# Optimization experiments

Hardware: AMD Instinct MI355X
Metric: run time of the kernel (lower is better)

## Reference

```python
import jax, jax.numpy as jnp
import numpy as np

N = 100000
E = 1600000
IN_C, HID_C, OUT_C = 128, 128, 64
EPS = 1e-5


def setup_inputs() -> dict:
    key = jax.random.key(0)
    ks = jax.random.split(key, 12)
    x = jax.random.normal(ks[0], (N, IN_C), dtype=jnp.float32)
    edge_index = jax.random.randint(ks[1], (2, E), 0, N, dtype=jnp.int64)
    def lin(k, fan_in, fan_out):
        s = 1.0 / np.sqrt(fan_in)
        return jax.random.uniform(k, (fan_in, fan_out), jnp.float32, -s, s)
    return {
        "x": x,
        "W1": lin(ks[2], IN_C, HID_C), "b1": jnp.zeros((HID_C,), jnp.float32),
        "g1": jnp.ones((HID_C,), jnp.float32), "be1": jnp.zeros((HID_C,), jnp.float32),
        "W2": lin(ks[3], HID_C, HID_C), "b2": jnp.zeros((HID_C,), jnp.float32),
        "g2": jnp.ones((HID_C,), jnp.float32), "be2": jnp.zeros((HID_C,), jnp.float32),
        "W3": lin(ks[4], HID_C, OUT_C), "b3": jnp.zeros((OUT_C,), jnp.float32),
        "edge_index": edge_index,
    }


def gcn_conv(x, W, b, src, dst, dinv):
    # x' = D^{-1/2}(A+I)D^{-1/2} (x W) + b ; src/dst already include self loops
    h = x @ W                                    # [N, C_out]
    norm = dinv[src] * dinv[dst]                 # [E+N]
    msg = h[src] * norm[:, None]                 # [E+N, C_out] (memory-bound gather)
    out = jax.ops.segment_sum(msg, dst, num_segments=N)
    return out + b


def batchnorm_relu(h, gamma, beta):
    # training-mode BatchNorm1d: batch stats over nodes, biased variance
    mean = jnp.mean(h, axis=0)
    var = jnp.mean((h - mean) ** 2, axis=0)
    y = gamma * (h - mean) * jax.lax.rsqrt(var + EPS) + beta
    return jax.nn.relu(y)


def reference(x, W1, b1, g1, be1, W2, b2, g2, be2, W3, b3, edge_index):
    loop = jnp.arange(N, dtype=edge_index.dtype)
    src = jnp.concatenate([edge_index[0], loop])
    dst = jnp.concatenate([edge_index[1], loop])
    deg = jax.ops.segment_sum(jnp.ones_like(dst, dtype=jnp.float32), dst, num_segments=N)
    dinv = jax.lax.rsqrt(jnp.maximum(deg, 1.0))

    h = gcn_conv(x, W1, b1, src, dst, dinv)
    h = batchnorm_relu(h, g1, be1)
    h = gcn_conv(h, W2, b2, src, dst, dinv)
    h = batchnorm_relu(h, g2, be2)
    out = gcn_conv(h, W3, b3, src, dst, dinv)
    return (h, out)
```

## Files before the change

kernel.cpp:

```cpp
#include <hip/hip_runtime.h>
#include <hip/hip_bf16.h>

#define NNODES 100000
#define NEDGES 1600000
#define EPSBN 1e-5f

#define BKT_SHIFT 9
#define NODES_PER_BKT 512
#define NBKT 196
#define NCHUNK 256
#define CHUNK 6250
#define SRC_MASK 0x1FFFF
#define NSLOT 64

typedef unsigned short u16;
typedef unsigned int u32;
typedef __bf16 bf16x8 __attribute__((ext_vector_type(8)));
typedef float floatx4 __attribute__((ext_vector_type(4)));

__device__ __forceinline__ u16 f2bf(float f) {
    unsigned int u = __float_as_uint(f);
    unsigned int r = (u + 0x7fffu + ((u >> 16) & 1u)) >> 16;
    return (u16)r;
}
__device__ __forceinline__ float bflo(unsigned int u) { return __uint_as_float(u << 16); }
__device__ __forceinline__ float bfhi(unsigned int u) { return __uint_as_float(u & 0xffff0000u); }


__global__ __launch_bounds__(256) void k_hist(const int* __restrict__ ei, int* __restrict__ histT) {
    __shared__ int h[NBKT];
    int tid = threadIdx.x;
    if (tid < NBKT) h[tid] = 0;
    __syncthreads();
    int base = blockIdx.x * CHUNK;
    for (int e = base + tid; e < base + CHUNK; e += 256) {
        int d = ei[NEDGES + e];
        atomicAdd(&h[d >> BKT_SHIFT], 1);
    }
    __syncthreads();
    if (tid < NBKT) histT[tid * NCHUNK + blockIdx.x] = h[tid];
}

__global__ __launch_bounds__(256) void k_bbase(const int* __restrict__ histT, int* __restrict__ bbase,
                                               int* __restrict__ rowptr) {
    __shared__ int sdata[256];
    int tid = threadIdx.x;
    int s = 0;
    if (tid < NBKT) {
        for (int g = 0; g < NCHUNK; ++g) s += histT[tid * NCHUNK + g];
    }
    int val = s;
    sdata[tid] = val;
    __syncthreads();
    for (int off = 1; off < 256; off <<= 1) {
        int add = (tid >= off) ? sdata[tid - off] : 0;
        __syncthreads();
        val += add;
        sdata[tid] = val;
        __syncthreads();
    }
    if (tid < NBKT) bbase[tid] = val - s;
    if (tid == 0) { bbase[NBKT] = NEDGES; rowptr[NNODES] = NEDGES; }
}

__global__ __launch_bounds__(256) void k_bscan(const int* __restrict__ histT, const int* __restrict__ bbase,
                                               int* __restrict__ offT) {
    __shared__ int sdata[256];
    int b = blockIdx.x;
    int g = threadIdx.x;
    int v = histT[b * NCHUNK + g];
    int val = v;
    sdata[g] = val;
    __syncthreads();
    for (int off = 1; off < 256; off <<= 1) {
        int add = (g >= off) ? sdata[g - off] : 0;
        __syncthreads();
        val += add;
        sdata[g] = val;
        __syncthreads();
    }
    offT[b * NCHUNK + g] = bbase[b] + (val - v);
}

__global__ __launch_bounds__(256) void k_scatter(const int* __restrict__ ei, const int* __restrict__ offT,
                                                 u32* __restrict__ rec) {
    __shared__ int cur[NBKT];
    int tid = threadIdx.x;
    if (tid < NBKT) cur[tid] = offT[tid * NCHUNK + blockIdx.x];
    __syncthreads();
    int base = blockIdx.x * CHUNK;
    for (int e = base + tid; e < base + CHUNK; e += 256) {
        int s = ei[e];
        int d = ei[NEDGES + e];
        int b = d >> BKT_SHIFT;
        int p = atomicAdd(&cur[b], 1);
        rec[p] = ((u32)(d & (NODES_PER_BKT - 1)) << 17) | (u32)s;
    }
}

__global__ __launch_bounds__(256) void k_bfill(const u32* __restrict__ rec, const int* __restrict__ bbase,
                                               int* __restrict__ rowptr, float* __restrict__ dinv,
                                               int* __restrict__ colsrc) {
    __shared__ int cnt[NODES_PER_BKT];
    __shared__ int sdata[256];
    int tid = threadIdx.x;
    int b = blockIdx.x;
    int n0 = b * NODES_PER_BKT;
    int r0 = bbase[b], r1 = bbase[b + 1];
    cnt[2 * tid] = 0;
    cnt[2 * tid + 1] = 0;
    __syncthreads();
    for (int r = r0 + tid; r < r1; r += 256) {
        atomicAdd(&cnt[rec[r] >> 17], 1);
    }
    __syncthreads();
    int c0 = cnt[2 * tid], c1 = cnt[2 * tid + 1];
    int ps = c0 + c1;
    int val = ps;
    sdata[tid] = val;
    __syncthreads();
    for (int off = 1; off < 256; off <<= 1) {
        int add = (tid >= off) ? sdata[tid - off] : 0;
        __syncthreads();
        val += add;
        sdata[tid] = val;
        __syncthreads();
    }
    int e0 = val - ps;
    int e1 = e0 + c0;
    int na = n0 + 2 * tid, nb2 = n0 + 2 * tid + 1;
    if (na < NNODES) {
        rowptr[na] = r0 + e0;
        dinv[na] = rsqrtf((float)(c0 + 1));
    }
    if (nb2 < NNODES) {
        rowptr[nb2] = r0 + e1;
        dinv[nb2] = rsqrtf((float)(c1 + 1));
    }
    cnt[2 * tid] = r0 + e0;
    cnt[2 * tid + 1] = r0 + e1;
    __syncthreads();
    for (int r = r0 + tid; r < r1; r += 256) {
        u32 u = rec[r];
        int p = atomicAdd(&cnt[u >> 17], 1);
        colsrc[p] = (int)(u & SRC_MASK);
    }
}


template <int COUT>
__device__ __forceinline__ void packone(const float* __restrict__ W, u16* __restrict__ Wp, int f) {
    constexpr int CT = COUT / 16;
    if (f >= 4 * CT * 64) return;
    int ks = f / (CT * 64);
    int ct = (f / 64) % CT;
    int lane = f % 64;
    int quad = lane >> 4, mm = lane & 15;
#pragma unroll
    for (int j = 0; j < 8; ++j) {
        float v = W[(size_t)(ks * 32 + quad * 8 + j) * COUT + ct * 16 + mm];
        Wp[(size_t)f * 8 + j] = f2bf(v);
    }
}

__global__ __launch_bounds__(256) void k_packW_all(const float* __restrict__ W1, const float* __restrict__ W2,
                                                   const float* __restrict__ W3, u16* __restrict__ Wp1,
                                                   u16* __restrict__ Wp2, u16* __restrict__ Wp3) {
    int b = blockIdx.x;
    if (b < 8) packone<128>(W1, Wp1, b * 256 + threadIdx.x);
    else if (b < 16) packone<128>(W2, Wp2, (b - 8) * 256 + threadIdx.x);
    else packone<64>(W3, Wp3, (b - 16) * 256 + threadIdx.x);
}


template <int COUT, bool AFFINE, bool WRITEH, bool BF16IN>
__global__ __launch_bounds__(256) void k_mfma_gemm(const void* __restrict__ Xv, const u16* __restrict__ Wp,
                                                   const float* __restrict__ dinv,
                                                   const float* __restrict__ scale, const float* __restrict__ shift,
                                                   u16* __restrict__ Bout, float* __restrict__ Hout) {
    constexpr int CT = COUT / 16;
    const int wave = threadIdx.x >> 6;
    const int lane = threadIdx.x & 63;
    const int quad = lane >> 4;
    const int m = lane & 15;
    const int rowbase = blockIdx.x * 64 + wave * 16;
    const int arow = rowbase + m;
    const bool rv = arow < NNODES;
    floatx4 acc[CT];
#pragma unroll
    for (int ct = 0; ct < CT; ++ct) acc[ct] = floatx4{0.f, 0.f, 0.f, 0.f};
#pragma unroll
    for (int ks = 0; ks < 4; ++ks) {
        const int k0 = ks * 32 + quad * 8;
        float4 xa = make_float4(0.f, 0.f, 0.f, 0.f), xb = xa;
        if (rv) {
            if (BF16IN) {
                uint4 q = *(const uint4*)((const u16*)Xv + (size_t)arow * 128 + k0);
                xa.x = bflo(q.x); xa.y = bfhi(q.x); xa.z = bflo(q.y); xa.w = bfhi(q.y);
                xb.x = bflo(q.z); xb.y = bfhi(q.z); xb.z = bflo(q.w); xb.w = bfhi(q.w);
            } else {
                xa = *(const float4*)((const float*)Xv + (size_t)arow * 128 + k0);
                xb = *(const float4*)((const float*)Xv + (size_t)arow * 128 + k0 + 4);
            }
        }
        if (AFFINE) {
            float4 sa = *(const float4*)(scale + k0), sb = *(const float4*)(scale + k0 + 4);
            float4 ha = *(const float4*)(shift + k0), hb = *(const float4*)(shift + k0 + 4);
            xa.x = fmaxf(fmaf(xa.x, sa.x, ha.x), 0.f);
            xa.y = fmaxf(fmaf(xa.y, sa.y, ha.y), 0.f);
            xa.z = fmaxf(fmaf(xa.z, sa.z, ha.z), 0.f);
            xa.w = fmaxf(fmaf(xa.w, sa.w, ha.w), 0.f);
            xb.x = fmaxf(fmaf(xb.x, sb.x, hb.x), 0.f);
            xb.y = fmaxf(fmaf(xb.y, sb.y, hb.y), 0.f);
            xb.z = fmaxf(fmaf(xb.z, sb.z, hb.z), 0.f);
            xb.w = fmaxf(fmaf(xb.w, sb.w, hb.w), 0.f);
        }
        if (WRITEH && rv) {
            *(float4*)(Hout + (size_t)arow * 128 + k0) = xa;
            *(float4*)(Hout + (size_t)arow * 128 + k0 + 4) = xb;
        }
        union { u16 h[8]; bf16x8 v; } ua;
        ua.h[0] = f2bf(xa.x); ua.h[1] = f2bf(xa.y); ua.h[2] = f2bf(xa.z); ua.h[3] = f2bf(xa.w);
        ua.h[4] = f2bf(xb.x); ua.h[5] = f2bf(xb.y); ua.h[6] = f2bf(xb.z); ua.h[7] = f2bf(xb.w);
#pragma unroll
        for (int ct = 0; ct < CT; ++ct) {
            uint4 bv = *(const uint4*)(Wp + ((size_t)(ks * CT + ct) * 64 + lane) * 8);
            bf16x8 b = *(const bf16x8*)&bv;
            acc[ct] = __builtin_amdgcn_mfma_f32_16x16x32_bf16(ua.v, b, acc[ct], 0, 0, 0);
        }
    }
    float dv[4];
#pragma unroll
    for (int reg = 0; reg < 4; ++reg) {
        int r = rowbase + quad * 4 + reg;
        dv[reg] = (r < NNODES) ? dinv[r] : 0.f;
    }
#pragma unroll
    for (int ct = 0; ct < CT; ++ct) {
#pragma unroll
        for (int reg = 0; reg < 4; ++reg) {
            int r = rowbase + quad * 4 + reg;
            if (r < NNODES) Bout[(size_t)r * COUT + ct * 16 + m] = f2bf(dv[reg] * acc[ct][reg]);
        }
    }
}


template <bool STATS, bool OUTB>
__global__ __launch_bounds__(256) void k_agg128v(const u16* __restrict__ Bm, const float* __restrict__ dinv,
                                                 const int* __restrict__ rowptr, const int* __restrict__ colsrc,
                                                 const float* __restrict__ bias, void* __restrict__ Outv,
                                                 float* __restrict__ slots) {
    __shared__ float sO[4][128];
    const int wave = threadIdx.x >> 6;
    const int node = blockIdx.x * 4 + wave;
    const int lane = threadIdx.x & 63;
    const int g = lane >> 4;
    const int c16 = lane & 15;
    const uint4* Bq = (const uint4*)Bm;
    float a0[8], a1[8];
#pragma unroll
    for (int j = 0; j < 8; ++j) { a0[j] = 0.f; a1[j] = 0.f; }
    const int beg = rowptr[node];
    const int L = rowptr[node + 1] - beg + 1;
    for (int it = 0; it < L; it += 8) {
        int i0 = it + g, i1 = it + 4 + g;
        float w0 = (i0 < L) ? 1.f : 0.f;
        float w1 = (i1 < L) ? 1.f : 0.f;
        i0 = min(i0, L - 1);
        i1 = min(i1, L - 1);
        int s0 = colsrc[beg + max(i0, 1) - 1];
        int s1 = colsrc[beg + max(i1, 1) - 1];
        if (i0 == 0) s0 = node;
        uint4 q0 = Bq[(size_t)s0 * 16 + c16];
        uint4 q1 = Bq[(size_t)s1 * 16 + c16];
        a0[0] += w0 * bflo(q0.x); a0[1] += w0 * bfhi(q0.x);
        a0[2] += w0 * bflo(q0.y); a0[3] += w0 * bfhi(q0.y);
        a0[4] += w0 * bflo(q0.z); a0[5] += w0 * bfhi(q0.z);
        a0[6] += w0 * bflo(q0.w); a0[7] += w0 * bfhi(q0.w);
        a1[0] += w1 * bflo(q1.x); a1[1] += w1 * bfhi(q1.x);
        a1[2] += w1 * bflo(q1.y); a1[3] += w1 * bfhi(q1.y);
        a1[4] += w1 * bflo(q1.z); a1[5] += w1 * bfhi(q1.z);
        a1[6] += w1 * bflo(q1.w); a1[7] += w1 * bfhi(q1.w);
    }
    const float dv = dinv[node];
    float o[8];
#pragma unroll
    for (int j = 0; j < 8; ++j) {
        float s = a0[j] + a1[j];
        s += __shfl_xor(s, 16);
        s += __shfl_xor(s, 32);
        o[j] = dv * s + bias[c16 * 8 + j];
    }
    if (g == 0) {
        if (OUTB) {
            u16* OutB = (u16*)Outv;
            union { u32 w[4]; uint4 q; } p;
            p.w[0] = (u32)f2bf(o[0]) | ((u32)f2bf(o[1]) << 16);
            p.w[1] = (u32)f2bf(o[2]) | ((u32)f2bf(o[3]) << 16);
            p.w[2] = (u32)f2bf(o[4]) | ((u32)f2bf(o[5]) << 16);
            p.w[3] = (u32)f2bf(o[6]) | ((u32)f2bf(o[7]) << 16);
            *(uint4*)(OutB + (size_t)node * 128 + c16 * 8) = p.q;
        } else {
            float* Out = (float*)Outv;
            *(float4*)(Out + (size_t)node * 128 + c16 * 8) = make_float4(o[0], o[1], o[2], o[3]);
            *(float4*)(Out + (size_t)node * 128 + c16 * 8 + 4) = make_float4(o[4], o[5], o[6], o[7]);
        }
        if (STATS) {
#pragma unroll
            for (int j = 0; j < 8; ++j) sO[wave][c16 * 8 + j] = o[j];
        }
    }
    if (STATS) {
        __syncthreads();
        if (threadIdx.x < 128) {
            float s = 0.f, q = 0.f;
#pragma unroll
            for (int wv = 0; wv < 4; ++wv) {
                float v = sO[wv][threadIdx.x];
                s += v;
                q += v * v;
            }
            float* slot = slots + (size_t)(blockIdx.x & (NSLOT - 1)) * 256;
            atomicAdd(&slot[threadIdx.x], s);
            atomicAdd(&slot[128 + threadIdx.x], q);
        }
    }
}

__global__ __launch_bounds__(256) void k_agg64v(const u16* __restrict__ Bm, const float* __restrict__ dinv,
                                                const int* __restrict__ rowptr, const int* __restrict__ colsrc,
                                                const float* __restrict__ bias, float* __restrict__ Out) {
    const int node = blockIdx.x * 4 + (threadIdx.x >> 6);
    const int lane = threadIdx.x & 63;
    const int g = lane >> 3;
    const int c8 = lane & 7;
    const uint4* Bq = (const uint4*)Bm;
    float a0[8], a1[8];
#pragma unroll
    for (int j = 0; j < 8; ++j) { a0[j] = 0.f; a1[j] = 0.f; }
    const int beg = rowptr[node];
    const int L = rowptr[node + 1] - beg + 1;
    for (int it = 0; it < L; it += 16) {
        int i0 = it + g, i1 = it + 8 + g;
        float w0 = (i0 < L) ? 1.f : 0.f;
        float w1 = (i1 < L) ? 1.f : 0.f;
        i0 = min(i0, L - 1);
        i1 = min(i1, L - 1);
        int s0 = colsrc[beg + max(i0, 1) - 1];
        int s1 = colsrc[beg + max(i1, 1) - 1];
        if (i0 == 0) s0 = node;
        uint4 q0 = Bq[(size_t)s0 * 8 + c8];
        uint4 q1 = Bq[(size_t)s1 * 8 + c8];
        a0[0] += w0 * bflo(q0.x); a0[1] += w0 * bfhi(q0.x);
        a0[2] += w0 * bflo(q0.y); a0[3] += w0 * bfhi(q0.y);
        a0[4] += w0 * bflo(q0.z); a0[5] += w0 * bfhi(q0.z);
        a0[6] += w0 * bflo(q0.w); a0[7] += w0 * bfhi(q0.w);
        a1[0] += w1 * bflo(q1.x); a1[1] += w1 * bfhi(q1.x);
        a1[2] += w1 * bflo(q1.y); a1[3] += w1 * bfhi(q1.y);
        a1[4] += w1 * bflo(q1.z); a1[5] += w1 * bfhi(q1.z);
        a1[6] += w1 * bflo(q1.w); a1[7] += w1 * bfhi(q1.w);
    }
    const float dv = dinv[node];
    float o[8];
#pragma unroll
    for (int j = 0; j < 8; ++j) {
        float s = a0[j] + a1[j];
        s += __shfl_xor(s, 8);
        s += __shfl_xor(s, 16);
        s += __shfl_xor(s, 32);
        o[j] = dv * s + bias[c8 * 8 + j];
    }
    if (g == 0) {
        float4 v0 = make_float4(o[0], o[1], o[2], o[3]);
        float4 v1 = make_float4(o[4], o[5], o[6], o[7]);
        *(float4*)(Out + (size_t)node * 64 + c8 * 8) = v0;
        *(float4*)(Out + (size_t)node * 64 + c8 * 8 + 4) = v1;
    }
}


__global__ void k_bn_final(const float* __restrict__ slots, const float* __restrict__ g,
                           const float* __restrict__ be, float* __restrict__ scale, float* __restrict__ shift) {
    int c = threadIdx.x;
    float s = 0.f, q = 0.f;
    for (int k = 0; k < NSLOT; ++k) {
        s += slots[(size_t)k * 256 + c];
        q += slots[(size_t)k * 256 + 128 + c];
    }
    float mean = s * (1.0f / NNODES);
    float var = q * (1.0f / NNODES) - mean * mean;
    float istd = rsqrtf(var + EPSBN);
    float sc = g[c] * istd;
    scale[c] = sc;
    shift[c] = be[c] - sc * mean;
}


extern "C" void kernel_launch(void* const* d_in, const int* in_sizes, int n_in,
                              void* d_out, int out_size, void* d_ws, size_t ws_size,
                              hipStream_t stream) {
    const float* x   = (const float*)d_in[0];
    const float* W1  = (const float*)d_in[1];
    const float* b1  = (const float*)d_in[2];
    const float* g1  = (const float*)d_in[3];
    const float* be1 = (const float*)d_in[4];
    const float* W2  = (const float*)d_in[5];
    const float* b2  = (const float*)d_in[6];
    const float* g2  = (const float*)d_in[7];
    const float* be2 = (const float*)d_in[8];
    const float* W3  = (const float*)d_in[9];
    const float* b3  = (const float*)d_in[10];
    const int* ei    = (const int*)d_in[11];

    float* out_h = (float*)d_out;
    float* out_o = (float*)d_out + (size_t)NNODES * 128;

    char* w = (char*)d_ws;
    u16* A16 = (u16*)w;        w += (size_t)NNODES * 128 * 2;
    u16* Bm = (u16*)w;         w += (size_t)NNODES * 128 * 2;
    float* dinv = (float*)w;   w += (size_t)NNODES * 4;
    int* rowptr = (int*)w;     w += (size_t)(NNODES + 32) * 4;
    int* colsrc = (int*)w;     w += (size_t)(NEDGES + 8) * 4;
    int* bbase = (int*)w;      w += (NBKT + 4) * 4;
    float* slots1 = (float*)w; w += (size_t)NSLOT * 256 * 4;
    float* slots2 = (float*)w; w += (size_t)NSLOT * 256 * 4;
    float* scale = (float*)w;  w += 128 * 4;
    float* shift = (float*)w;  w += 128 * 4;
    u16* Wp1 = (u16*)w;        w += 128 * 128 * 2;
    u16* Wp2 = (u16*)w;        w += 128 * 128 * 2;
    u16* Wp3 = (u16*)w;        w += 128 * 64 * 2;

    u32* rec  = (u32*)A16;
    int* histT = (int*)Bm;
    int* offT  = (int*)Bm + NBKT * NCHUNK;

    hipMemsetAsync(slots1, 0, (size_t)2 * NSLOT * 256 * 4, stream);

    k_packW_all<<<20, 256, 0, stream>>>(W1, W2, W3, Wp1, Wp2, Wp3);

    k_hist<<<NCHUNK, 256, 0, stream>>>(ei, histT);
    k_bbase<<<1, 256, 0, stream>>>(histT, bbase, rowptr);
    k_bscan<<<NBKT, 256, 0, stream>>>(histT, bbase, offT);
    k_scatter<<<NCHUNK, 256, 0, stream>>>(ei, offT, rec);
    k_bfill<<<NBKT, 256, 0, stream>>>(rec, bbase, rowptr, dinv, colsrc);

    const int GB = (NNODES + 63) / 64;
    const int AB = NNODES / 4;

    k_mfma_gemm<128, false, false, false><<<GB, 256, 0, stream>>>(x, Wp1, dinv, nullptr, nullptr, Bm, nullptr);
    k_agg128v<true, true><<<AB, 256, 0, stream>>>(Bm, dinv, rowptr, colsrc, b1, A16, slots1);
    k_bn_final<<<1, 128, 0, stream>>>(slots1, g1, be1, scale, shift);

    k_mfma_gemm<128, true, false, true><<<GB, 256, 0, stream>>>(A16, Wp2, dinv, scale, shift, Bm, nullptr);
    k_agg128v<true, true><<<AB, 256, 0, stream>>>(Bm, dinv, rowptr, colsrc, b2, A16, slots2);
    k_bn_final<<<1, 128, 0, stream>>>(slots2, g2, be2, scale, shift);

    k_mfma_gemm<64, true, true, true><<<GB, 256, 0, stream>>>(A16, Wp3, dinv, scale, shift, Bm, out_h);
    k_agg64v<<<AB, 256, 0, stream>>>(Bm, dinv, rowptr, colsrc, b3, out_o);
}
```

Baseline: 452.6 us.

## Pre-sort edges by source bucket before destination bucketing for gather locality

Adds a first counting-sort pass that buckets edges by source node into an intermediate (src,dst) pair array, then runs the existing destination bucketing over that array. Because the destination scatter is stable per chunk, each node's CSR neighbor list ends up roughly ordered by source, which should make the feature-row gathers in the aggregation kernels more cache-local. It costs four extra kernel launches and an extra pass of edge reads and writes over an 8-byte-per-edge staging buffer.

```diff
diff --git a/kernel.cpp b/kernel.cpp
--- a/kernel.cpp
+++ b/kernel.cpp
@@ -27,14 +27,65 @@
 __device__ __forceinline__ float bfhi(unsigned int u) { return __uint_as_float(u & 0xffff0000u); }
 
 
-__global__ __launch_bounds__(256) void k_hist(const int* __restrict__ ei, int* __restrict__ histT) {
+__global__ __launch_bounds__(256) void k_histS(const int* __restrict__ ei, int* __restrict__ histS) {
     __shared__ int h[NBKT];
     int tid = threadIdx.x;
     if (tid < NBKT) h[tid] = 0;
     __syncthreads();
     int base = blockIdx.x * CHUNK;
     for (int e = base + tid; e < base + CHUNK; e += 256) {
+        int s = ei[e];
+        atomicAdd(&h[s >> BKT_SHIFT], 1);
+    }
+    __syncthreads();
+    if (tid < NBKT) histS[tid * NCHUNK + blockIdx.x] = h[tid];
+}
+
+__global__ __launch_bounds__(256) void k_bbaseS(const int* __restrict__ histS, int* __restrict__ bbaseS) {
+    __shared__ int sdata[256];
+    int tid = threadIdx.x;
+    int s = 0;
+    if (tid < NBKT) {
+        for (int g = 0; g < NCHUNK; ++g) s += histS[tid * NCHUNK + g];
+    }
+    int val = s;
+    sdata[tid] = val;
+    __syncthreads();
+    for (int off = 1; off < 256; off <<= 1) {
+        int add = (tid >= off) ? sdata[tid - off] : 0;
+        __syncthreads();
+        val += add;
+        sdata[tid] = val;
+        __syncthreads();
+    }
+    if (tid < NBKT) bbaseS[tid] = val - s;
+}
+
+__global__ __launch_bounds__(256) void k_scatterS(const int* __restrict__ ei, const int* __restrict__ offS,
+                                                  uint2* __restrict__ est) {
+    __shared__ int cur[NBKT];
+    int tid = threadIdx.x;
+    if (tid < NBKT) cur[tid] = offS[tid * NCHUNK + blockIdx.x];
+    __syncthreads();
+    int base = blockIdx.x * CHUNK;
+    for (int e = base + tid; e < base + CHUNK; e += 256) {
+        int s = ei[e];
         int d = ei[NEDGES + e];
+        int b = s >> BKT_SHIFT;
+        int p = atomicAdd(&cur[b], 1);
+        est[p] = make_uint2((u32)s, (u32)d);
+    }
+}
+
+
+__global__ __launch_bounds__(256) void k_hist(const uint2* __restrict__ est, int* __restrict__ histT) {
+    __shared__ int h[NBKT];
+    int tid = threadIdx.x;
+    if (tid < NBKT) h[tid] = 0;
+    __syncthreads();
+    int base = blockIdx.x * CHUNK;
+    for (int e = base + tid; e < base + CHUNK; e += 256) {
+        int d = (int)est[e].y;
         atomicAdd(&h[d >> BKT_SHIFT], 1);
     }
     __syncthreads();
@@ -82,7 +133,7 @@
     offT[b * NCHUNK + g] = bbase[b] + (val - v);
 }
 
-__global__ __launch_bounds__(256) void k_scatter(const int* __restrict__ ei, const int* __restrict__ offT,
+__global__ __launch_bounds__(256) void k_scatter(const uint2* __restrict__ est, const int* __restrict__ offT,
                                                  u32* __restrict__ rec) {
     __shared__ int cur[NBKT];
     int tid = threadIdx.x;
@@ -90,8 +141,9 @@
     __syncthreads();
     int base = blockIdx.x * CHUNK;
     for (int e = base + tid; e < base + CHUNK; e += 256) {
-        int s = ei[e];
-        int d = ei[NEDGES + e];
+        uint2 p2 = est[e];
+        int s = (int)p2.x;
+        int d = (int)p2.y;
         int b = d >> BKT_SHIFT;
         int p = atomicAdd(&cur[b], 1);
         rec[p] = ((u32)(d & (NODES_PER_BKT - 1)) << 17) | (u32)s;
@@ -423,6 +475,7 @@
     int* rowptr = (int*)w;     w += (size_t)(NNODES + 32) * 4;
     int* colsrc = (int*)w;     w += (size_t)(NEDGES + 8) * 4;
     int* bbase = (int*)w;      w += (NBKT + 4) * 4;
+    int* bbaseS = (int*)w;     w += (NBKT + 4) * 4;
     float* slots1 = (float*)w; w += (size_t)NSLOT * 256 * 4;
     float* slots2 = (float*)w; w += (size_t)NSLOT * 256 * 4;
     float* scale = (float*)w;  w += 128 * 4;
@@ -432,17 +485,25 @@
     u16* Wp3 = (u16*)w;        w += 128 * 64 * 2;
 
     u32* rec  = (u32*)A16;
+    uint2* est = (uint2*)((char*)A16 + (size_t)NEDGES * 4);
     int* histT = (int*)Bm;
-    int* offT  = (int*)Bm + NBKT * NCHUNK;
+    int* offT  = histT + NBKT * NCHUNK;
+    int* histS = offT + NBKT * NCHUNK;
+    int* offS  = histS + NBKT * NCHUNK;
 
     hipMemsetAsync(slots1, 0, (size_t)2 * NSLOT * 256 * 4, stream);
 
     k_packW_all<<<20, 256, 0, stream>>>(W1, W2, W3, Wp1, Wp2, Wp3);
 
-    k_hist<<<NCHUNK, 256, 0, stream>>>(ei, histT);
+    k_histS<<<NCHUNK, 256, 0, stream>>>(ei, histS);
+    k_bbaseS<<<1, 256, 0, stream>>>(histS, bbaseS);
+    k_bscan<<<NBKT, 256, 0, stream>>>(histS, bbaseS, offS);
+    k_scatterS<<<NCHUNK, 256, 0, stream>>>(ei, offS, est);
+
+    k_hist<<<NCHUNK, 256, 0, stream>>>(est, histT);
     k_bbase<<<1, 256, 0, stream>>>(histT, bbase, rowptr);
     k_bscan<<<NBKT, 256, 0, stream>>>(histT, bbase, offT);
-    k_scatter<<<NCHUNK, 256, 0, stream>>>(ei, offT, rec);
+    k_scatter<<<NCHUNK, 256, 0, stream>>>(est, offT, rec);
     k_bfill<<<NBKT, 256, 0, stream>>>(rec, bbase, rowptr, dinv, colsrc);
 
     const int GB = (NNODES + 63) / 64;
```

After: 484.6 us. +7.1%, slower.
